# Kernel tuning notes

Hardware: AMD Instinct MI355X
Metric: run time of the kernel (lower is better)

The kernel has to match this reference:

```python
import jax, jax.numpy as jnp
import numpy as np

B, T, F, H, O = 64, 500, 89, 512, 72


def setup_inputs() -> dict:
    key = jax.random.key(0)
    ks = jax.random.split(key, 16)
    d = {
        "batch": jax.random.normal(ks[0], (B, T, F), dtype=jnp.float32),
        "lengths": jax.random.randint(ks[1], (B,), 250, T + 1),
    }
    in_sizes = [F, 2 * H, 2 * H]  # layer 0 takes features, layers 1-2 take bidir output
    for i, fi in enumerate(in_sizes):
        d[f"w{i}"] = jax.random.normal(ks[2 + 3 * i], (2 * H, fi), dtype=jnp.float32) / np.sqrt(fi).astype(np.float32)
        d[f"b{i}"] = jnp.zeros((2 * H,), jnp.float32)
        d[f"u{i}"] = jax.random.normal(ks[3 + 3 * i], (2 * H, H), dtype=jnp.float32) / np.sqrt(H).astype(np.float32)
    d["wfc"] = jax.random.normal(ks[12], (O, 2 * H), dtype=jnp.float32) / np.sqrt(2 * H).astype(np.float32)
    d["bfc"] = jnp.zeros((O,), jnp.float32)
    return d


def _ligru_bidir(x, W, b, U):
    # SpeechBrain LiGRU layer: fwd and bwd directions share weights; the
    # time-flipped copy is stacked along the batch dim and one scan is run.
    Bx = x.shape[0]
    xb = jnp.concatenate([x, x[:, ::-1]], axis=0)            # [2B, T, in]
    gates_x = jnp.einsum('btf,gf->tbg', xb, W) + b           # [T, 2B, 2H] precomputed input gates
    h0 = jnp.zeros((2 * Bx, H), x.dtype)

    def step(h, g):
        g = g + h @ U.T                                       # [2B, 2H]
        at, zt = jnp.split(g, 2, axis=-1)
        zt = jax.nn.sigmoid(zt)
        h = zt * h + (1.0 - zt) * jnp.tanh(at)                # nonlinearity='tanh'
        return h, h

    _, hs = jax.lax.scan(step, h0, gates_x)                   # [T, 2B, H]
    hs = jnp.swapaxes(hs, 0, 1)                               # [2B, T, H]
    return jnp.concatenate([hs[:Bx], hs[Bx:, ::-1]], axis=2)  # [B, T, 2H]


def reference(batch, lengths, w0, b0, u0, w1, b1, u1, w2, b2, u2, wfc, bfc):
    x = batch
    for W, b, U in ((w0, b0, u0), (w1, b1, u1), (w2, b2, u2)):
        x = _ligru_bidir(x, W, b, U)
    out = jnp.einsum('bth,oh->bto', x, wfc) + bfc             # [B, T, O]
    # Pack valid frames per utterance: predictions[p:p+len_i] = out[i, :len_i]
    mask = (jnp.arange(T)[None, :] < lengths[:, None]).ravel()  # [B*T]
    order = jnp.argsort(jnp.logical_not(mask), stable=True)     # valid rows first, in order
    total = int(np.asarray(lengths).sum())
    return out.reshape(B * T, O)[order][:total]
```

## Files before the change

### kernel.cpp

```cpp
#include <hip/hip_runtime.h>

typedef _Float16 f16;
typedef _Float16 half8 __attribute__((ext_vector_type(8)));
typedef float f32x4 __attribute__((ext_vector_type(4)));

__device__ inline float frcp(float x) {
#if __has_builtin(__builtin_amdgcn_rcpf)
  return __builtin_amdgcn_rcpf(x);
#else
  return 1.0f / x;
#endif
}
__device__ inline float fexp2(float x) {
#if __has_builtin(__builtin_amdgcn_exp2f)
  return __builtin_amdgcn_exp2f(x);
#else
  return exp2f(x);
#endif
}

__device__ inline unsigned int pack2f16(float a, float b) {
  f16 x = (f16)a, y = (f16)b;
  unsigned short ux = __builtin_bit_cast(unsigned short, x);
  unsigned short uy = __builtin_bit_cast(unsigned short, y);
  return (unsigned int)ux | ((unsigned int)uy << 16);
}


__global__ void k_cvt(const float* __restrict__ s, f16* __restrict__ d, int n) {
  int i = blockIdx.x * 256 + threadIdx.x;
  if (i < n) d[i] = (f16)s[i];
}

__global__ void k_zero(unsigned int* __restrict__ p, int n) {
  int i = blockIdx.x * 256 + threadIdx.x;
  if (i < n) p[i] = 0u;
}

__global__ void k_w0pad(const float* __restrict__ w0, f16* __restrict__ d) {
  int i = blockIdx.x * 256 + threadIdx.x;
  if (i >= 1024 * 96) return;
  int row = i / 96, c = i % 96;
  d[i] = (c < 89) ? (f16)w0[row * 89 + c] : (f16)0.f;
}

__global__ void k_xb0(const float* __restrict__ x, f16* __restrict__ d) {
  int i = blockIdx.x * 256 + threadIdx.x;
  if (i >= 128 * 500 * 96) return;
  int f = i % 96;
  int t = (i / 96) % 500;
  int s = i / (96 * 500);
  float v = 0.f;
  if (f < 89) {
    if (s < 64) v = x[((size_t)s * 500 + t) * 89 + f];
    else        v = x[((size_t)(s - 64) * 500 + (499 - t)) * 89 + f];
  }
  d[i] = (f16)v;
}

__global__ void k_offs(const int* __restrict__ lens, int* __restrict__ offs) {
  if (threadIdx.x == 0 && blockIdx.x == 0) {
    int s = 0;
    for (int i = 0; i < 64; ++i) { offs[i] = s; s += lens[i]; }
  }
}

template <int MODE>
__global__ __launch_bounds__(256) void k_gates(const f16* __restrict__ Aw,
                                               const f16* __restrict__ W16,
                                               const float* __restrict__ bias,
                                               f16* __restrict__ gates) {
  constexpr int KW = MODE ? 1024 : 96;
  const int t = blockIdx.x;
  const int nb = blockIdx.y * 128;
  const int tid = threadIdx.x;
  const int w = tid >> 6, l = tid & 63, c = l & 15, rg = l >> 4;
  const int wr = w >> 1, wc = w & 1;

  __shared__ f16 As[128 * 40];
  __shared__ f16 Bs[128 * 40];

  f32x4 acc[4][4] = {};

  const int srow = tid >> 1;
  const int seg = (tid & 1) * 16;

  for (int kb = 0; kb < KW; kb += 32) {
    const f16* pa;
    if (MODE == 0) {
      pa = Aw + ((size_t)srow * 500 + t) * 96 + kb + seg;
    } else {
      int f0 = kb + seg;
      int half = f0 >> 9;
      int col = f0 & 511;
      int s = srow;
      int seq, time;
      if (s < 64) { seq = half ? 64 + s : s;  time = half ? 499 - t : t; }
      else        { seq = half ? s : s - 64;  time = half ? t : 499 - t; }
      pa = Aw + ((size_t)seq * 500 + time) * 512 + col;
    }
    const f16* pb = W16 + (size_t)(nb + srow) * KW + kb + seg;
    half8 a0 = *(const half8*)pa;
    half8 a1 = *(const half8*)(pa + 8);
    half8 b0 = *(const half8*)pb;
    half8 b1 = *(const half8*)(pb + 8);
    __syncthreads();
    *(half8*)&As[srow * 40 + seg] = a0;
    *(half8*)&As[srow * 40 + seg + 8] = a1;
    *(half8*)&Bs[srow * 40 + seg] = b0;
    *(half8*)&Bs[srow * 40 + seg + 8] = b1;
    __syncthreads();
    half8 aF[4], bF[4];
#pragma unroll
    for (int i = 0; i < 4; ++i)
      aF[i] = *(const half8*)&As[(wr * 64 + i * 16 + c) * 40 + rg * 8];
#pragma unroll
    for (int j = 0; j < 4; ++j)
      bF[j] = *(const half8*)&Bs[(wc * 64 + j * 16 + c) * 40 + rg * 8];
#pragma unroll
    for (int i = 0; i < 4; ++i)
#pragma unroll
      for (int j = 0; j < 4; ++j)
        acc[i][j] = __builtin_amdgcn_mfma_f32_16x16x32_f16(aF[i], bF[j], acc[i][j], 0, 0, 0);
  }

#pragma unroll
  for (int j = 0; j < 4; ++j) {
    int n = nb + wc * 64 + j * 16 + c;
    float bj = bias[n];
#pragma unroll
    for (int i = 0; i < 4; ++i) {
#pragma unroll
      for (int r = 0; r < 4; ++r) {
        int m = wr * 64 + i * 16 + rg * 4 + r;
        gates[((size_t)t * 128 + m) * 1024 + n] = (f16)(acc[i][j][r] + bj);
      }
    }
  }
}

__global__ __launch_bounds__(256, 1) void k_rec(const f16* __restrict__ gates,
                                                const f16* __restrict__ U,
                                                f16* __restrict__ hs,
                                                float* __restrict__ hx,
                                                unsigned int* __restrict__ cnt) {
  const int sg = blockIdx.x & 7, cg = blockIdx.x >> 3;
  const int tid = threadIdx.x;
  const int l = tid & 63, w = tid >> 6, c = l & 15, rg = l >> 4;
  const int s0 = sg * 16;
  const int hcol = cg * 64 + w * 16;
  const int an0 = hcol, zn0 = 512 + hcol;

  __shared__ f16 hlds[16 * 512];

  half8 ua[16], uz[16];
#pragma unroll
  for (int kt = 0; kt < 16; ++kt) {
    ua[kt] = *(const half8*)(U + (size_t)(an0 + c) * 512 + kt * 32 + rg * 8);
    uz[kt] = *(const half8*)(U + (size_t)(zn0 + c) * 512 + kt * 32 + rg * 8);
  }

  float hold[4] = {0.f, 0.f, 0.f, 0.f};
  unsigned int* cflag = cnt + sg * 32;

  f16 ga[4], gz[4];
  {
    const f16* gb = gates + ((size_t)0 * 128 + s0 + rg * 4) * 1024;
#pragma unroll
    for (int r = 0; r < 4; ++r) { ga[r] = gb[r * 1024 + an0 + c]; gz[r] = gb[r * 1024 + zn0 + c]; }
  }

  for (int t = 0; t < 500; ++t) {
    int tn = (t + 1 < 500) ? t + 1 : 499;
    f16 gna[4], gnz[4];
    {
      const f16* gb = gates + ((size_t)tn * 128 + s0 + rg * 4) * 1024;
#pragma unroll
      for (int r = 0; r < 4; ++r) { gna[r] = gb[r * 1024 + an0 + c]; gnz[r] = gb[r * 1024 + zn0 + c]; }
    }

    if (t) {
      const unsigned int tgt = 32u * (unsigned int)t;
      int guard = 0;
      while (__hip_atomic_load(cflag, __ATOMIC_RELAXED, __HIP_MEMORY_SCOPE_AGENT) < tgt) {
        if (++guard > (1 << 17)) break;
      }
      asm volatile("" ::: "memory");
    }

    {
      const int p0 = t & 1;
      const unsigned long long* hsrc =
          (const unsigned long long*)(hx + (size_t)p0 * 65536 + (size_t)s0 * 512);
      unsigned long long tmp[16];
#pragma unroll
      for (int n = 0; n < 16; ++n)
        tmp[n] = __hip_atomic_load(hsrc + n * 256 + tid, __ATOMIC_RELAXED, __HIP_MEMORY_SCOPE_AGENT);
#pragma unroll
      for (int n = 0; n < 16; ++n) {
        float lo = __builtin_bit_cast(float, (unsigned int)tmp[n]);
        float hi = __builtin_bit_cast(float, (unsigned int)(tmp[n] >> 32));
        int elem = (n * 512 + tid * 2) ^ ((n & 7) << 3);
        *(unsigned int*)&hlds[elem] = pack2f16(lo, hi);
      }
    }
    __syncthreads();

    f32x4 acc_a, acc_z;
#pragma unroll
    for (int r = 0; r < 4; ++r) { acc_a[r] = (float)ga[r]; acc_z[r] = (float)gz[r]; }
#pragma unroll
    for (int kt = 0; kt < 16; ++kt) {
      int elem = (c * 512 + kt * 32 + rg * 8) ^ ((c & 7) << 3);
      half8 aF = *(const half8*)&hlds[elem];
      acc_a = __builtin_amdgcn_mfma_f32_16x16x32_f16(aF, ua[kt], acc_a, 0, 0, 0);
      acc_z = __builtin_amdgcn_mfma_f32_16x16x32_f16(aF, uz[kt], acc_z, 0, 0, 0);
    }

    const int p1 = (t & 1) ^ 1;
    float* hdst = hx + (size_t)p1 * 65536;
#pragma unroll
    for (int r = 0; r < 4; ++r) {
      float av = acc_a[r];
      float zv = acc_z[r];
      float zs = frcp(1.f + fexp2(-1.44269504f * zv));
      float u2 = fexp2(2.88539008f * av);
      float th = 1.f - 2.f * frcp(u2 + 1.f);
      float hn = th + zs * (hold[r] - th);
      hold[r] = hn;
      int srow = rg * 4 + r;
      __hip_atomic_store(&hdst[(size_t)(s0 + srow) * 512 + hcol + c], hn,
                         __ATOMIC_RELAXED, __HIP_MEMORY_SCOPE_AGENT);
      hs[((size_t)(s0 + srow) * 500 + t) * 512 + hcol + c] = (f16)hn;
    }

    asm volatile("s_waitcnt vmcnt(0)" ::: "memory");
    if (l == 0)
      __hip_atomic_fetch_add(cflag, 1u, __ATOMIC_RELAXED, __HIP_MEMORY_SCOPE_AGENT);

#pragma unroll
    for (int r = 0; r < 4; ++r) { ga[r] = gna[r]; gz[r] = gnz[r]; }
  }
}

__global__ __launch_bounds__(256) void k_fc(const f16* __restrict__ hs,
                                            const f16* __restrict__ wfc,
                                            const float* __restrict__ bfc,
                                            const int* __restrict__ lens,
                                            const int* __restrict__ offs,
                                            float* __restrict__ out) {
  const int b = blockIdx.x, chunk = blockIdx.y;
  const int tid = threadIdx.x;
  __shared__ f16 X[16][1032];
#pragma unroll
  for (int ii = 0; ii < 8; ++ii) {
    int sg = ii * 256 + tid;
    int row = sg >> 7;
    int f = (sg & 127) * 8;
    int t = chunk * 16 + row;
    int tt = t < 500 ? t : 499;
    int half = f >> 9, col = f & 511;
    int seq = half ? 64 + b : b;
    int time = half ? 499 - tt : tt;
    *(half8*)&X[row][f] = *(const half8*)&hs[((size_t)seq * 500 + time) * 512 + col];
  }
  __syncthreads();
  int row = tid >> 4, og = tid & 15;
  int t = chunk * 16 + row;
  int len = lens[b];
  float acc[5];
#pragma unroll
  for (int j = 0; j < 5; ++j) {
    int o = j * 16 + og;
    acc[j] = (o < 72) ? bfc[o] : 0.f;
  }
  for (int k8 = 0; k8 < 128; ++k8) {
    half8 x8 = *(const half8*)&X[row][k8 * 8];
    float xf[8];
#pragma unroll
    for (int e = 0; e < 8; ++e) xf[e] = (float)x8[e];
#pragma unroll
    for (int j = 0; j < 5; ++j) {
      int o = j * 16 + og;
      int oc = o < 72 ? o : 0;
      half8 w8 = *(const half8*)&wfc[(size_t)oc * 1024 + k8 * 8];
#pragma unroll
      for (int e = 0; e < 8; ++e) acc[j] += xf[e] * (float)w8[e];
    }
  }
  if (t < 500 && t < len) {
    size_t base = ((size_t)offs[b] + t) * 72;
#pragma unroll
    for (int j = 0; j < 5; ++j) {
      int o = j * 16 + og;
      if (o < 72) out[base + o] = acc[j];
    }
  }
}


extern "C" void kernel_launch(void* const* d_in, const int* in_sizes, int n_in,
                              void* d_out, int out_size, void* d_ws, size_t ws_size,
                              hipStream_t stream) {
  const float* batch = (const float*)d_in[0];
  const int*   lens  = (const int*)d_in[1];
  const float* w0 = (const float*)d_in[2];
  const float* b0 = (const float*)d_in[3];
  const float* u0 = (const float*)d_in[4];
  const float* w1 = (const float*)d_in[5];
  const float* b1 = (const float*)d_in[6];
  const float* u1 = (const float*)d_in[7];
  const float* w2 = (const float*)d_in[8];
  const float* b2 = (const float*)d_in[9];
  const float* u2 = (const float*)d_in[10];
  const float* wfc = (const float*)d_in[11];
  const float* bfc = (const float*)d_in[12];
  float* out = (float*)d_out;

  char* ws = (char*)d_ws;
  const size_t GATES_OFF = 0;
  const size_t HS_OFF    = 131072000;
  const size_t XB0_OFF   = 196608000;
  const size_t W0P_OFF   = 208896000;
  const size_t W1_OFF    = 209092608;
  const size_t W2_OFF    = 211189760;
  const size_t U0_OFF    = 213286912;
  const size_t U1_OFF    = 214335488;
  const size_t U2_OFF    = 215384064;
  const size_t WFC_OFF   = 216432640;
  const size_t OFFS_OFF  = 216580096;
  const size_t HX_OFF    = 216581120;
  const size_t CNT_OFF   = 217105408;

  f16* g_gates = (f16*)(ws + GATES_OFF);
  f16* g_hs    = (f16*)(ws + HS_OFF);
  f16* g_xb0   = (f16*)(ws + XB0_OFF);
  f16* g_w0p   = (f16*)(ws + W0P_OFF);
  f16* g_w1    = (f16*)(ws + W1_OFF);
  f16* g_w2    = (f16*)(ws + W2_OFF);
  f16* g_u0    = (f16*)(ws + U0_OFF);
  f16* g_u1    = (f16*)(ws + U1_OFF);
  f16* g_u2    = (f16*)(ws + U2_OFF);
  f16* g_wfc   = (f16*)(ws + WFC_OFF);
  int* g_offs  = (int*)(ws + OFFS_OFF);
  float* g_hx  = (float*)(ws + HX_OFF);
  unsigned int* g_cnt = (unsigned int*)(ws + CNT_OFF);
  unsigned int* g_sync0 = (unsigned int*)(ws + HX_OFF);
  const int ZERO_N = (524288 + 1024) / 4;

  hipLaunchKernelGGL(k_offs, dim3(1), dim3(64), 0, stream, lens, g_offs);

  auto cvt = [&](const float* s, f16* d, int n) {
    hipLaunchKernelGGL(k_cvt, dim3((n + 255) / 256), dim3(256), 0, stream, s, d, n);
  };
  cvt(w1, g_w1, 1024 * 1024);
  cvt(w2, g_w2, 1024 * 1024);
  cvt(u0, g_u0, 1024 * 512);
  cvt(u1, g_u1, 1024 * 512);
  cvt(u2, g_u2, 1024 * 512);
  cvt(wfc, g_wfc, 72 * 1024);
  hipLaunchKernelGGL(k_w0pad, dim3((1024 * 96 + 255) / 256), dim3(256), 0, stream, w0, g_w0p);
  hipLaunchKernelGGL(k_xb0, dim3((128 * 500 * 96 + 255) / 256), dim3(256), 0, stream, batch, g_xb0);

  hipLaunchKernelGGL((k_gates<0>), dim3(500, 8), dim3(256), 0, stream, g_xb0, g_w0p, b0, g_gates);
  hipLaunchKernelGGL(k_zero, dim3((ZERO_N + 255) / 256), dim3(256), 0, stream, g_sync0, ZERO_N);
  hipLaunchKernelGGL(k_rec, dim3(64), dim3(256), 0, stream, g_gates, g_u0, g_hs, g_hx, g_cnt);
  hipLaunchKernelGGL((k_gates<1>), dim3(500, 8), dim3(256), 0, stream, g_hs, g_w1, b1, g_gates);
  hipLaunchKernelGGL(k_zero, dim3((ZERO_N + 255) / 256), dim3(256), 0, stream, g_sync0, ZERO_N);
  hipLaunchKernelGGL(k_rec, dim3(64), dim3(256), 0, stream, g_gates, g_u1, g_hs, g_hx, g_cnt);
  hipLaunchKernelGGL((k_gates<1>), dim3(500, 8), dim3(256), 0, stream, g_hs, g_w2, b2, g_gates);
  hipLaunchKernelGGL(k_zero, dim3((ZERO_N + 255) / 256), dim3(256), 0, stream, g_sync0, ZERO_N);
  hipLaunchKernelGGL(k_rec, dim3(64), dim3(256), 0, stream, g_gates, g_u2, g_hs, g_hx, g_cnt);

  hipLaunchKernelGGL(k_fc, dim3(64, 32), dim3(256), 0, stream, g_hs, g_wfc, bfc, lens, g_offs, out);
}
```

Before: 4.908 ms.

## Replace counter barrier with tagged fp16 hidden-state words in recurrence

```diff
diff --git a/kernel.cpp b/kernel.cpp
--- a/kernel.cpp
+++ b/kernel.cpp
@@ -3,6 +3,8 @@
 typedef _Float16 f16;
 typedef _Float16 half8 __attribute__((ext_vector_type(8)));
 typedef float f32x4 __attribute__((ext_vector_type(4)));
+typedef unsigned int u32;
+typedef u32 u32x4 __attribute__((ext_vector_type(4)));
 
 __device__ inline float frcp(float x) {
 #if __has_builtin(__builtin_amdgcn_rcpf)
@@ -19,20 +21,13 @@
 #endif
 }
 
-__device__ inline unsigned int pack2f16(float a, float b) {
-  f16 x = (f16)a, y = (f16)b;
-  unsigned short ux = __builtin_bit_cast(unsigned short, x);
-  unsigned short uy = __builtin_bit_cast(unsigned short, y);
-  return (unsigned int)ux | ((unsigned int)uy << 16);
-}
-
 
 __global__ void k_cvt(const float* __restrict__ s, f16* __restrict__ d, int n) {
   int i = blockIdx.x * 256 + threadIdx.x;
   if (i < n) d[i] = (f16)s[i];
 }
 
-__global__ void k_zero(unsigned int* __restrict__ p, int n) {
+__global__ void k_zero(u32* __restrict__ p, int n) {
   int i = blockIdx.x * 256 + threadIdx.x;
   if (i < n) p[i] = 0u;
 }
@@ -77,13 +72,15 @@
   const int w = tid >> 6, l = tid & 63, c = l & 15, rg = l >> 4;
   const int wr = w >> 1, wc = w & 1;
 
-  __shared__ f16 As[128 * 40];
-  __shared__ f16 Bs[128 * 40];
+  __shared__ f16 As[128 * 32];
+  __shared__ f16 Bs[128 * 32];
 
   f32x4 acc[4][4] = {};
 
   const int srow = tid >> 1;
   const int seg = (tid & 1) * 16;
+  const int ch0 = seg >> 3;
+  const int wsw = (srow >> 1) & 3;
 
   for (int kb = 0; kb < KW; kb += 32) {
     const f16* pa;
@@ -105,18 +102,22 @@
     half8 b0 = *(const half8*)pb;
     half8 b1 = *(const half8*)(pb + 8);
     __syncthreads();
-    *(half8*)&As[srow * 40 + seg] = a0;
-    *(half8*)&As[srow * 40 + seg + 8] = a1;
-    *(half8*)&Bs[srow * 40 + seg] = b0;
-    *(half8*)&Bs[srow * 40 + seg + 8] = b1;
+    *(half8*)&As[srow * 32 + ((ch0 + 0) ^ wsw) * 8] = a0;
+    *(half8*)&As[srow * 32 + ((ch0 + 1) ^ wsw) * 8] = a1;
+    *(half8*)&Bs[srow * 32 + ((ch0 + 0) ^ wsw) * 8] = b0;
+    *(half8*)&Bs[srow * 32 + ((ch0 + 1) ^ wsw) * 8] = b1;
     __syncthreads();
     half8 aF[4], bF[4];
 #pragma unroll
-    for (int i = 0; i < 4; ++i)
-      aF[i] = *(const half8*)&As[(wr * 64 + i * 16 + c) * 40 + rg * 8];
-#pragma unroll
-    for (int j = 0; j < 4; ++j)
-      bF[j] = *(const half8*)&Bs[(wc * 64 + j * 16 + c) * 40 + rg * 8];
+    for (int i = 0; i < 4; ++i) {
+      int row = wr * 64 + i * 16 + c;
+      aF[i] = *(const half8*)&As[row * 32 + ((rg ^ ((row >> 1) & 3)) * 8)];
+    }
+#pragma unroll
+    for (int j = 0; j < 4; ++j) {
+      int row = wc * 64 + j * 16 + c;
+      bF[j] = *(const half8*)&Bs[row * 32 + ((rg ^ ((row >> 1) & 3)) * 8)];
+    }
 #pragma unroll
     for (int i = 0; i < 4; ++i)
 #pragma unroll
@@ -142,8 +143,8 @@
 __global__ __launch_bounds__(256, 1) void k_rec(const f16* __restrict__ gates,
                                                 const f16* __restrict__ U,
                                                 f16* __restrict__ hs,
-                                                float* __restrict__ hx,
-                                                unsigned int* __restrict__ cnt) {
+                                                u32* __restrict__ hx,
+                                                int tagbase) {
   const int sg = blockIdx.x & 7, cg = blockIdx.x >> 3;
   const int tid = threadIdx.x;
   const int l = tid & 63, w = tid >> 6, c = l & 15, rg = l >> 4;
@@ -159,9 +160,13 @@
     ua[kt] = *(const half8*)(U + (size_t)(an0 + c) * 512 + kt * 32 + rg * 8);
     uz[kt] = *(const half8*)(U + (size_t)(zn0 + c) * 512 + kt * 32 + rg * 8);
   }
+#pragma unroll
+  for (int kt = 0; kt < 16; ++kt) {
+    asm volatile("" : "+v"(ua[kt]));
+    asm volatile("" : "+v"(uz[kt]));
+  }
 
   float hold[4] = {0.f, 0.f, 0.f, 0.f};
-  unsigned int* cflag = cnt + sg * 32;
 
   f16 ga[4], gz[4];
   {
@@ -179,30 +184,47 @@
       for (int r = 0; r < 4; ++r) { gna[r] = gb[r * 1024 + an0 + c]; gnz[r] = gb[r * 1024 + zn0 + c]; }
     }
 
-    if (t) {
-      const unsigned int tgt = 32u * (unsigned int)t;
+    u32x4 vv[8];
+    if (t == 0) {
+#pragma unroll
+      for (int v = 0; v < 8; ++v) vv[v] = (u32x4){0u, 0u, 0u, 0u};
+    } else {
+      const u32 exp = (u32)(tagbase + t);
+      const u32* hsrc = hx + (size_t)(t & 1) * 65536 + (size_t)s0 * 512 + tid * 4;
+      unsigned mask = 0xffu;
       int guard = 0;
-      while (__hip_atomic_load(cflag, __ATOMIC_RELAXED, __HIP_MEMORY_SCOPE_AGENT) < tgt) {
-        if (++guard > (1 << 17)) break;
+      while (mask) {
+#pragma unroll
+        for (int v = 0; v < 8; ++v) {
+          if (mask & (1u << v)) {
+            u32 a  = __hip_atomic_load(hsrc + v * 1024 + 0, __ATOMIC_RELAXED, __HIP_MEMORY_SCOPE_AGENT);
+            u32 b  = __hip_atomic_load(hsrc + v * 1024 + 1, __ATOMIC_RELAXED, __HIP_MEMORY_SCOPE_AGENT);
+            u32 cc = __hip_atomic_load(hsrc + v * 1024 + 2, __ATOMIC_RELAXED, __HIP_MEMORY_SCOPE_AGENT);
+            u32 dd = __hip_atomic_load(hsrc + v * 1024 + 3, __ATOMIC_RELAXED, __HIP_MEMORY_SCOPE_AGENT);
+            vv[v] = (u32x4){a, b, cc, dd};
+          }
+        }
+#pragma unroll
+        for (int v = 0; v < 8; ++v) {
+          if (mask & (1u << v)) {
+            if ((vv[v].x >> 16) == exp && (vv[v].y >> 16) == exp &&
+                (vv[v].z >> 16) == exp && (vv[v].w >> 16) == exp)
+              mask &= ~(1u << v);
+          }
+        }
+        if (++guard > (1 << 14)) break;
       }
-      asm volatile("" ::: "memory");
-    }
-
-    {
-      const int p0 = t & 1;
-      const unsigned long long* hsrc =
-          (const unsigned long long*)(hx + (size_t)p0 * 65536 + (size_t)s0 * 512);
-      unsigned long long tmp[16];
-#pragma unroll
-      for (int n = 0; n < 16; ++n)
-        tmp[n] = __hip_atomic_load(hsrc + n * 256 + tid, __ATOMIC_RELAXED, __HIP_MEMORY_SCOPE_AGENT);
-#pragma unroll
-      for (int n = 0; n < 16; ++n) {
-        float lo = __builtin_bit_cast(float, (unsigned int)tmp[n]);
-        float hi = __builtin_bit_cast(float, (unsigned int)(tmp[n] >> 32));
-        int elem = (n * 512 + tid * 2) ^ ((n & 7) << 3);
-        *(unsigned int*)&hlds[elem] = pack2f16(lo, hi);
-      }
+    }
+
+#pragma unroll
+    for (int v = 0; v < 8; ++v) {
+      int elem = v * 1024 + tid * 4;
+      int row = elem >> 9, col = elem & 511;
+      u32 d0 = (vv[v].x & 0xffffu) | (vv[v].y << 16);
+      u32 d1 = (vv[v].z & 0xffffu) | (vv[v].w << 16);
+      int idx = (row * 512 + col) ^ ((row & 7) << 3);
+      unsigned long long dd = (unsigned long long)d0 | ((unsigned long long)d1 << 32);
+      *(unsigned long long*)&hlds[idx] = dd;
     }
     __syncthreads();
 
@@ -217,8 +239,9 @@
       acc_z = __builtin_amdgcn_mfma_f32_16x16x32_f16(aF, uz[kt], acc_z, 0, 0, 0);
     }
 
-    const int p1 = (t & 1) ^ 1;
-    float* hdst = hx + (size_t)p1 * 65536;
+    const u32 tagn = (u32)(tagbase + t + 1);
+    u32* hdst = hx + (size_t)((t + 1) & 1) * 65536;
+    float hnv[4];
 #pragma unroll
     for (int r = 0; r < 4; ++r) {
       float av = acc_a[r];
@@ -228,15 +251,14 @@
       float th = 1.f - 2.f * frcp(u2 + 1.f);
       float hn = th + zs * (hold[r] - th);
       hold[r] = hn;
-      int srow = rg * 4 + r;
-      __hip_atomic_store(&hdst[(size_t)(s0 + srow) * 512 + hcol + c], hn,
+      hnv[r] = hn;
+      u32 word = (u32)__builtin_bit_cast(unsigned short, (f16)hn) | (tagn << 16);
+      __hip_atomic_store(&hdst[(size_t)(s0 + rg * 4 + r) * 512 + hcol + c], word,
                          __ATOMIC_RELAXED, __HIP_MEMORY_SCOPE_AGENT);
-      hs[((size_t)(s0 + srow) * 500 + t) * 512 + hcol + c] = (f16)hn;
-    }
-
-    asm volatile("s_waitcnt vmcnt(0)" ::: "memory");
-    if (l == 0)
-      __hip_atomic_fetch_add(cflag, 1u, __ATOMIC_RELAXED, __HIP_MEMORY_SCOPE_AGENT);
+    }
+#pragma unroll
+    for (int r = 0; r < 4; ++r)
+      hs[((size_t)(s0 + rg * 4 + r) * 500 + t) * 512 + hcol + c] = (f16)hnv[r];
 
 #pragma unroll
     for (int r = 0; r < 4; ++r) { ga[r] = gna[r]; gz[r] = gnz[r]; }
@@ -330,7 +352,6 @@
   const size_t WFC_OFF   = 216432640;
   const size_t OFFS_OFF  = 216580096;
   const size_t HX_OFF    = 216581120;
-  const size_t CNT_OFF   = 217105408;
 
   f16* g_gates = (f16*)(ws + GATES_OFF);
   f16* g_hs    = (f16*)(ws + HS_OFF);
@@ -343,10 +364,7 @@
   f16* g_u2    = (f16*)(ws + U2_OFF);
   f16* g_wfc   = (f16*)(ws + WFC_OFF);
   int* g_offs  = (int*)(ws + OFFS_OFF);
-  float* g_hx  = (float*)(ws + HX_OFF);
-  unsigned int* g_cnt = (unsigned int*)(ws + CNT_OFF);
-  unsigned int* g_sync0 = (unsigned int*)(ws + HX_OFF);
-  const int ZERO_N = (524288 + 1024) / 4;
+  u32* g_hx    = (u32*)(ws + HX_OFF);
 
   hipLaunchKernelGGL(k_offs, dim3(1), dim3(64), 0, stream, lens, g_offs);
 
@@ -361,16 +379,14 @@
   cvt(wfc, g_wfc, 72 * 1024);
   hipLaunchKernelGGL(k_w0pad, dim3((1024 * 96 + 255) / 256), dim3(256), 0, stream, w0, g_w0p);
   hipLaunchKernelGGL(k_xb0, dim3((128 * 500 * 96 + 255) / 256), dim3(256), 0, stream, batch, g_xb0);
+  hipLaunchKernelGGL(k_zero, dim3(512), dim3(256), 0, stream, g_hx, 131072);
 
   hipLaunchKernelGGL((k_gates<0>), dim3(500, 8), dim3(256), 0, stream, g_xb0, g_w0p, b0, g_gates);
-  hipLaunchKernelGGL(k_zero, dim3((ZERO_N + 255) / 256), dim3(256), 0, stream, g_sync0, ZERO_N);
-  hipLaunchKernelGGL(k_rec, dim3(64), dim3(256), 0, stream, g_gates, g_u0, g_hs, g_hx, g_cnt);
+  hipLaunchKernelGGL(k_rec, dim3(64), dim3(256), 0, stream, g_gates, g_u0, g_hs, g_hx, 0);
   hipLaunchKernelGGL((k_gates<1>), dim3(500, 8), dim3(256), 0, stream, g_hs, g_w1, b1, g_gates);
-  hipLaunchKernelGGL(k_zero, dim3((ZERO_N + 255) / 256), dim3(256), 0, stream, g_sync0, ZERO_N);
-  hipLaunchKernelGGL(k_rec, dim3(64), dim3(256), 0, stream, g_gates, g_u1, g_hs, g_hx, g_cnt);
+  hipLaunchKernelGGL(k_rec, dim3(64), dim3(256), 0, stream, g_gates, g_u1, g_hs, g_hx, 512);
   hipLaunchKernelGGL((k_gates<1>), dim3(500, 8), dim3(256), 0, stream, g_hs, g_w2, b2, g_gates);
-  hipLaunchKernelGGL(k_zero, dim3((ZERO_N + 255) / 256), dim3(256), 0, stream, g_sync0, ZERO_N);
-  hipLaunchKernelGGL(k_rec, dim3(64), dim3(256), 0, stream, g_gates, g_u2, g_hs, g_hx, g_cnt);
+  hipLaunchKernelGGL(k_rec, dim3(64), dim3(256), 0, stream, g_gates, g_u2, g_hs, g_hx, 1024);
 
   hipLaunchKernelGGL(k_fc, dim3(64, 32), dim3(256), 0, stream, g_hs, g_wfc, bfc, lens, g_offs, out);
 }
```

Result: slower. 6.758 ms (+37.7%).
